# Kernel optimization log

Hardware: AMD Instinct MI355X
Metric: run time of the kernel (lower is better)

The kernel has to match this reference:

```python
import jax, jax.numpy as jnp
import numpy as np

B, D_IN, H, LAT = 4096, 4096, 4096, 512


def setup_inputs() -> dict:
    key = jax.random.key(0)
    ks = jax.random.split(key, 10)
    s = lambda fan_in: 1.0 / np.sqrt(fan_in)
    return {
        "x": jax.random.normal(ks[0], (B, D_IN), jnp.float32),
        "W_e1": jax.random.normal(ks[1], (D_IN, H), jnp.float32) * s(D_IN),
        "b_e1": jax.random.uniform(ks[2], (H,), jnp.float32),
        "W_e2": jax.random.normal(ks[3], (H, 2 * LAT), jnp.float32) * s(H),
        "b_e2": jax.random.uniform(ks[4], (2 * LAT,), jnp.float32),
        "W_d1": jax.random.normal(ks[5], (LAT, H), jnp.float32) * s(LAT),
        "b_d1": jax.random.uniform(ks[6], (H,), jnp.float32),
        "W_d2": jax.random.normal(ks[7], (H, D_IN), jnp.float32) * s(H),
        "b_d2": jax.random.uniform(ks[8], (D_IN,), jnp.float32),
        "eps": jax.random.normal(ks[9], (B, LAT), jnp.float32),
    }


def reference(x, W_e1, b_e1, W_e2, b_e2, W_d1, b_d1, W_d2, b_d2, eps):
    # encoder MLP
    h = jax.nn.relu(x @ W_e1 + b_e1)
    z = h @ W_e2 + b_e2                      # [B, 2*LAT]
    mu, logvar = z[:, :LAT], z[:, LAT:]
    # reparameterize: cholesky(diag(exp(logvar))) @ eps + mu == exp(0.5*logvar)*eps + mu
    zs = mu + jnp.exp(0.5 * logvar) * eps    # [B, LAT]
    # decoder MLP
    hd = jax.nn.relu(zs @ W_d1 + b_d1)
    recon = hd @ W_d2 + b_d2                 # [B, D_IN]
    return recon, mu, logvar
```

## Files before the change

### kernel.cpp

```cpp
#include <hip/hip_runtime.h>
#include <hip/hip_bf16.h>

typedef __attribute__((ext_vector_type(8))) __bf16 bf16x8;
typedef __attribute__((ext_vector_type(4))) float f32x4;
typedef __attribute__((ext_vector_type(4))) unsigned short ushort4v;
typedef __attribute__((ext_vector_type(8))) unsigned short ushort8v;
typedef unsigned short u16;

__device__ __forceinline__ u16 f2bf_bits(float f) {
    union { float f; unsigned int u; } x; x.f = f;
    unsigned int r = x.u + 0x7FFFu + ((x.u >> 16) & 1u);
    return (u16)(r >> 16);
}

__device__ __forceinline__ float bf2f(u16 u) {
    union { unsigned int i; float f; } x; x.i = ((unsigned)u) << 16; return x.f;
}

__device__ __forceinline__ void gload_lds16(const void* g, void* l) {
    __builtin_amdgcn_global_load_lds(
        (const __attribute__((address_space(1))) void*)g,
        (__attribute__((address_space(3))) void*)l, 16, 0, 0);
}

#define BARRIER()  __builtin_amdgcn_s_barrier()
#define LGKM0()    asm volatile("s_waitcnt lgkmcnt(0)" ::: "memory")
#define VMW8()     asm volatile("s_waitcnt vmcnt(8)" ::: "memory")

__global__ __launch_bounds__(256)
void prep(const float* __restrict__ x,   u16* __restrict__ xb,
          const float* __restrict__ We1, u16* __restrict__ w1t,
          const float* __restrict__ We2, u16* __restrict__ w2t,
          const float* __restrict__ Wd1, u16* __restrict__ w3t,
          const float* __restrict__ Wd2, u16* __restrict__ w4t) {
    int bid = blockIdx.x;

    if (bid >= 9728) {
        const int i = ((bid - 9728) << 10) + ((int)threadIdx.x << 2);
        f32x4 v = *reinterpret_cast<const f32x4*>(x + i);
        ushort4v o;
        o.x = f2bf_bits(v.x); o.y = f2bf_bits(v.y);
        o.z = f2bf_bits(v.z); o.w = f2bf_bits(v.w);
        *reinterpret_cast<ushort4v*>(xb + i) = o;
        return;
    }

    const float* in; u16* out; int R, C, bx, by;
    if (bid < 4096)      { in = We1; out = w1t; R = 4096; C = 4096; bx = bid & 63; by = bid >> 6; }
    else if (bid < 5120) { bid -= 4096; in = We2; out = w2t; R = 4096; C = 1024; bx = bid & 15; by = bid >> 4; }
    else if (bid < 5632) { bid -= 5120; in = Wd1; out = w3t; R = 512;  C = 4096; bx = bid & 63; by = bid >> 6; }
    else                 { bid -= 5632; in = Wd2; out = w4t; R = 4096; C = 4096; bx = bid & 63; by = bid >> 6; }

    __shared__ float t[64][67];
    const int c0 = bx << 6;
    const int r0 = by << 6;
    const int tx = threadIdx.x & 15;
    const int ty = threadIdx.x >> 4;
    #pragma unroll
    for (int j = 0; j < 4; ++j) {
        f32x4 v = *reinterpret_cast<const f32x4*>(
            &in[(size_t)(r0 + ty + 16 * j) * C + c0 + (tx << 2)]);
        *reinterpret_cast<f32x4*>(&t[ty + 16 * j][tx << 2]) = v;
    }
    __syncthreads();
    const int orow8 = threadIdx.x >> 3;
    const int seg8  = (threadIdx.x & 7) << 3;
    #pragma unroll
    for (int p = 0; p < 2; ++p) {
        const int oc = orow8 + (p << 5);
        ushort8v o;
        #pragma unroll
        for (int i = 0; i < 8; ++i)
            o[i] = f2bf_bits(t[seg8 + i][oc]);
        *reinterpret_cast<ushort8v*>(&out[(size_t)(c0 + oc) * R + r0 + seg8]) = o;
    }
}

__global__ __launch_bounds__(256)
void zred(const u16* __restrict__ P, const float* __restrict__ be2,
          const float* __restrict__ eps, float* __restrict__ mu,
          float* __restrict__ lv, u16* __restrict__ zs) {
    const int i = blockIdx.x * 256 + threadIdx.x;
    const int r = i >> 7;
    const int c4 = (i & 127) << 2;
    const size_t base = (size_t)r * 1024 + c4;
    const size_t PS = (size_t)4096 * 1024;

    f32x4 m = (f32x4)(0.0f);
    f32x4 l = (f32x4)(0.0f);
    #pragma unroll
    for (int s = 0; s < 4; ++s) {
        ushort4v pm = *reinterpret_cast<const ushort4v*>(P + s * PS + base);
        ushort4v pl = *reinterpret_cast<const ushort4v*>(P + s * PS + base + 512);
        m.x += bf2f(pm.x); m.y += bf2f(pm.y); m.z += bf2f(pm.z); m.w += bf2f(pm.w);
        l.x += bf2f(pl.x); l.y += bf2f(pl.y); l.z += bf2f(pl.z); l.w += bf2f(pl.w);
    }
    m += *reinterpret_cast<const f32x4*>(be2 + c4);
    l += *reinterpret_cast<const f32x4*>(be2 + 512 + c4);

    const size_t ob = (size_t)r * 512 + c4;
    *reinterpret_cast<f32x4*>(mu + ob) = m;
    *reinterpret_cast<f32x4*>(lv + ob) = l;

    f32x4 e = *reinterpret_cast<const f32x4*>(eps + ob);
    ushort4v o;
    o.x = f2bf_bits(m.x + __expf(0.5f * l.x) * e.x);
    o.y = f2bf_bits(m.y + __expf(0.5f * l.y) * e.y);
    o.z = f2bf_bits(m.z + __expf(0.5f * l.z) * e.z);
    o.w = f2bf_bits(m.w + __expf(0.5f * l.w) * e.w);
    *reinterpret_cast<ushort4v*>(zs + ob) = o;
}

template<int MODE, int PRIO>
__global__ __launch_bounds__(512, 2)
void gemm256(const u16* __restrict__ A, const u16* __restrict__ Bt,
             const float* __restrict__ bias,
             u16* __restrict__ obf, float* __restrict__ of32,
             int M, int N, int K, int ntiles)
{
    extern __shared__ char lds[];
    const int tid  = threadIdx.x;
    const int lane = tid & 63;
    const int w    = tid >> 6;
    const int wr   = w >> 2;
    const int wc   = w & 3;

    int bid = blockIdx.x;
    int sid = 0;
    int nwg = gridDim.x;
    if (MODE == 3) { sid = bid & 3; bid >>= 2; nwg >>= 2; }
    const int cpx = nwg >> 3;
    bid = (bid & 7) * cpx + (bid >> 3);
    const int nbx  = N >> 8;
    const int brow = (bid / nbx) << 8;
    const int bcol = (bid % nbx) << 8;
    const int kbase = (MODE == 3) ? sid * ntiles : 0;
    u16* pp = (MODE == 3) ? obf + (size_t)sid * M * N : obf;

    const int srow  = tid >> 3;
    const int scole = (((tid & 7) ^ (srow & 7)) << 4) >> 1;
    const size_t aoff = (size_t)(brow + srow) * K + scole;
    const size_t boff = (size_t)(bcol + srow) * K + scole;
    const size_t rowK64 = (size_t)64 * K;
    const int wave1024 = w << 10;

    const int lo16 = (lane >> 4) << 4;
    const int swzm = (lane & 7) << 4;
    const int low0 = lo16 ^ swzm;
    const int low1 = (64 | lo16) ^ swzm;
    const int rA   = (lane & 15) << 7;
    const int rB   = ((((wc & 1) << 6) | (lane & 15)) << 7);
    const int regA = wr << 14;
    const int regB = 32768 + ((wc >> 1) << 14);

    bf16x8 a[4][2];
    bf16x8 b0[2][2];
    bf16x8 b1[2][2];
    f32x4 acc[8][4];
    #pragma unroll
    for (int m = 0; m < 8; ++m)
        #pragma unroll
        for (int n = 0; n < 4; ++n)
            acc[m][n] = (f32x4)(0.0f);

#define STAGE_A(buf, h, kt) do { \
    const u16* _s = A + aoff + (size_t)(h) * 128 * K + (size_t)(kt) * 64; \
    gload_lds16(_s,          lds + ((buf) << 16) + ((h) << 14) + wave1024); \
    gload_lds16(_s + rowK64, lds + ((buf) << 16) + ((h) << 14) + 8192 + wave1024); \
} while (0)

#define STAGE_B(buf, h, kt) do { \
    const u16* _s = Bt + boff + (size_t)(h) * 128 * K + (size_t)(kt) * 64; \
    gload_lds16(_s,          lds + ((buf) << 16) + 32768 + ((h) << 14) + wave1024); \
    gload_lds16(_s + rowK64, lds + ((buf) << 16) + 32768 + ((h) << 14) + 8192 + wave1024); \
} while (0)

#define READ_A(buf, g) do { \
    _Pragma("unroll") \
    for (int m = 0; m < 4; ++m) { \
        const int _b = ((buf) << 16) + regA + rA + ((((g) << 2) + m) << 11); \
        a[m][0] = *reinterpret_cast<const bf16x8*>(lds + _b + low0); \
        a[m][1] = *reinterpret_cast<const bf16x8*>(lds + _b + low1); \
    } \
} while (0)

#define READ_B0(buf) do { \
    _Pragma("unroll") \
    for (int n = 0; n < 2; ++n) { \
        const int _b = ((buf) << 16) + regB + rB + (n << 11); \
        b0[n][0] = *reinterpret_cast<const bf16x8*>(lds + _b + low0); \
        b0[n][1] = *reinterpret_cast<const bf16x8*>(lds + _b + low1); \
    } \
} while (0)

#define READ_B1(buf) do { \
    _Pragma("unroll") \
    for (int n = 0; n < 2; ++n) { \
        const int _b = ((buf) << 16) + regB + rB + ((n + 2) << 11); \
        b1[n][0] = *reinterpret_cast<const bf16x8*>(lds + _b + low0); \
        b1[n][1] = *reinterpret_cast<const bf16x8*>(lds + _b + low1); \
    } \
} while (0)

#define MM(bx, mb, nb) do { \
    if (PRIO) __builtin_amdgcn_s_setprio(1); \
    _Pragma("unroll") \
    for (int m = 0; m < 4; ++m) \
        _Pragma("unroll") \
        for (int n = 0; n < 2; ++n) \
            _Pragma("unroll") \
            for (int s = 0; s < 2; ++s) \
                acc[(mb) + m][(nb) + n] = __builtin_amdgcn_mfma_f32_16x16x32_bf16( \
                    a[m][s], bx[n][s], acc[(mb) + m][(nb) + n], 0, 0, 0); \
    if (PRIO) __builtin_amdgcn_s_setprio(0); \
} while (0)

    const int NIT = ntiles >> 1;

    STAGE_A(0, 0, kbase); STAGE_A(0, 1, kbase); STAGE_B(0, 0, kbase); STAGE_B(0, 1, kbase);
    STAGE_A(1, 0, kbase + 1); STAGE_A(1, 1, kbase + 1); STAGE_B(1, 0, kbase + 1); STAGE_B(1, 1, kbase + 1);
    VMW8(); BARRIER();
    READ_A(0, 0); READ_B0(0);

    for (int it = 0; it < NIT; ++it) {
        const int tn0r = 2 * it + 2;
        const int tn1r = 2 * it + 3;
        const int tn0 = kbase + (tn0r < ntiles ? tn0r : ntiles - 1);
        const int tn1 = kbase + (tn1r < ntiles ? tn1r : ntiles - 1);

        BARRIER(); LGKM0();
        MM(b0, 0, 0);
        READ_B1(0);

        BARRIER(); LGKM0();
        STAGE_B(0, 0, tn0);
        MM(b1, 0, 2);
        READ_A(0, 1);

        BARRIER(); LGKM0();
        STAGE_B(0, 1, tn0);
        MM(b1, 4, 2);

        BARRIER(); LGKM0();
        STAGE_A(0, 0, tn0); STAGE_A(0, 1, tn0);
        MM(b0, 4, 0);
        VMW8();
        READ_A(1, 0); READ_B0(1);

        BARRIER(); LGKM0();
        MM(b0, 0, 0);
        READ_B1(1);

        BARRIER(); LGKM0();
        STAGE_B(1, 0, tn1);
        MM(b1, 0, 2);
        READ_A(1, 1);

        BARRIER(); LGKM0();
        STAGE_B(1, 1, tn1);
        MM(b1, 4, 2);

        BARRIER(); LGKM0();
        STAGE_A(1, 0, tn1); STAGE_A(1, 1, tn1);
        MM(b0, 4, 0);
        VMW8();
        READ_A(0, 0); READ_B0(0);
    }

    float bb[4];
    #pragma unroll
    for (int n = 0; n < 4; ++n)
        bb[n] = (MODE == 3) ? 0.0f : bias[bcol + (wc << 6) + (n << 4) + (lane & 15)];

    const int erow0 = brow + (wr << 7) + ((lane >> 4) << 2);
    const int ecol0 = bcol + (wc << 6) + (lane & 15);

    #pragma unroll
    for (int m = 0; m < 8; ++m) {
        #pragma unroll
        for (int i = 0; i < 4; ++i) {
            const int r = erow0 + (m << 4) + i;
            #pragma unroll
            for (int n = 0; n < 4; ++n) {
                const int c = ecol0 + (n << 4);
                float v = acc[m][n][i] + bb[n];
                if (MODE == 0) {
                    v = v > 0.0f ? v : 0.0f;
                    obf[(size_t)r * N + c] = f2bf_bits(v);
                } else if (MODE == 3) {
                    pp[(size_t)r * N + c] = f2bf_bits(v);
                } else {
                    of32[(size_t)r * N + c] = v;
                }
            }
        }
    }
#undef STAGE_A
#undef STAGE_B
#undef READ_A
#undef READ_B0
#undef READ_B1
#undef MM
}

extern "C" void kernel_launch(void* const* d_in, const int* in_sizes, int n_in,
                              void* d_out, int out_size, void* d_ws, size_t ws_size,
                              hipStream_t stream) {
    const float* x   = (const float*)d_in[0];
    const float* We1 = (const float*)d_in[1];
    const float* be1 = (const float*)d_in[2];
    const float* We2 = (const float*)d_in[3];
    const float* be2 = (const float*)d_in[4];
    const float* Wd1 = (const float*)d_in[5];
    const float* bd1 = (const float*)d_in[6];
    const float* Wd2 = (const float*)d_in[7];
    const float* bd2 = (const float*)d_in[8];
    const float* eps = (const float*)d_in[9];

    const int B = 4096, D = 4096, H = 4096, LAT = 512;

    char* ws = (char*)d_ws;
    u16*   xb    = (u16*)(ws);
    u16*   w1t   = (u16*)(ws + 33554432);
    u16*   w2t   = (u16*)(ws + 67108864);
    u16*   w3t   = (u16*)(ws + 75497472);
    u16*   w4t   = (u16*)(ws + 79691776);
    u16*   h     = (u16*)(ws + 113246208);
    u16*   part  = (u16*)(ws);
    u16*   zs    = (u16*)(ws + 113246208);
    u16*   hd    = (u16*)(ws);

    float* recon = (float*)d_out;
    float* mu    = recon + (size_t)B * D;
    float* lv    = mu + (size_t)B * LAT;

    hipFuncSetAttribute(reinterpret_cast<const void*>(gemm256<0, 0>),
                        hipFuncAttributeMaxDynamicSharedMemorySize, 131072);
    hipFuncSetAttribute(reinterpret_cast<const void*>(gemm256<0, 1>),
                        hipFuncAttributeMaxDynamicSharedMemorySize, 131072);
    hipFuncSetAttribute(reinterpret_cast<const void*>(gemm256<1, 1>),
                        hipFuncAttributeMaxDynamicSharedMemorySize, 131072);
    hipFuncSetAttribute(reinterpret_cast<const void*>(gemm256<3, 1>),
                        hipFuncAttributeMaxDynamicSharedMemorySize, 131072);

    prep<<<26112, 256, 0, stream>>>(x, xb, We1, w1t, We2, w2t, Wd1, w3t, Wd2, w4t);

    gemm256<0, 0><<<(B / 256) * (H / 256), 512, 131072, stream>>>(
        xb, w1t, be1, h, nullptr, B, H, D, D / 64);
    gemm256<3, 1><<<(B / 256) * (2 * LAT / 256) * 4, 512, 131072, stream>>>(
        h, w2t, nullptr, part, nullptr, B, 2 * LAT, H, (H / 64) / 4);
    zred<<<(B * LAT / 4) / 256, 256, 0, stream>>>(part, be2, eps, mu, lv, zs);
    gemm256<0, 1><<<(B / 256) * (H / 256), 512, 131072, stream>>>(
        zs, w3t, bd1, hd, nullptr, B, H, LAT, LAT / 64);
    gemm256<1, 1><<<(B / 256) * (D / 256), 512, 131072, stream>>>(
        hd, w4t, bd2, nullptr, recon, B, D, H, H / 64);
}
```

Measured before the change: 347.6 us.

## Double-buffer GEMM register fragments and interleave LDS reads with MFMAs

Fragment registers for A and B are duplicated so each phase can issue the LDS reads for the next phase before running its MFMAs, and sched_group_barrier hints ask the compiler to interleave DS reads with MFMA groups. The global-load wait is moved earlier and tightened to vmcnt(2), and the priority toggle is now applied to every GEMM, removing the PRIO template parameter. The aim is to hide LDS read latency behind matrix math. The extra fragment registers raise VGPR pressure at two blocks per CU, which may cause spills.

Result: slower. 418.1 us (+20.3%).

```diff
diff --git a/kernel.cpp b/kernel.cpp
--- a/kernel.cpp
+++ b/kernel.cpp
@@ -26,6 +26,9 @@
 #define BARRIER()  __builtin_amdgcn_s_barrier()
 #define LGKM0()    asm volatile("s_waitcnt lgkmcnt(0)" ::: "memory")
 #define VMW8()     asm volatile("s_waitcnt vmcnt(8)" ::: "memory")
+#define VMW2()     asm volatile("s_waitcnt vmcnt(2)" ::: "memory")
+#define SGB_DS(n)   __builtin_amdgcn_sched_group_barrier(0x100, n, 0)
+#define SGB_MFMA(n) __builtin_amdgcn_sched_group_barrier(0x8, n, 0)
 
 __global__ __launch_bounds__(256)
 void prep(const float* __restrict__ x,   u16* __restrict__ xb,
@@ -111,7 +114,7 @@
     *reinterpret_cast<ushort4v*>(zs + ob) = o;
 }
 
-template<int MODE, int PRIO>
+template<int MODE>
 __global__ __launch_bounds__(512, 2)
 void gemm256(const u16* __restrict__ A, const u16* __restrict__ Bt,
              const float* __restrict__ bias,
@@ -153,9 +156,9 @@
     const int regA = wr << 14;
     const int regB = 32768 + ((wc >> 1) << 14);
 
-    bf16x8 a[4][2];
-    bf16x8 b0[2][2];
-    bf16x8 b1[2][2];
+    bf16x8 aa0[4][2], aa1[4][2];
+    bf16x8 b0A[2][2], b0B[2][2];
+    bf16x8 b1A[2][2], b1B[2][2];
     f32x4 acc[8][4];
     #pragma unroll
     for (int m = 0; m < 8; ++m)
@@ -175,35 +178,26 @@
     gload_lds16(_s + rowK64, lds + ((buf) << 16) + 32768 + ((h) << 14) + 8192 + wave1024); \
 } while (0)
 
-#define READ_A(buf, g) do { \
+#define READ_AF(dst, buf, g) do { \
     _Pragma("unroll") \
     for (int m = 0; m < 4; ++m) { \
         const int _b = ((buf) << 16) + regA + rA + ((((g) << 2) + m) << 11); \
-        a[m][0] = *reinterpret_cast<const bf16x8*>(lds + _b + low0); \
-        a[m][1] = *reinterpret_cast<const bf16x8*>(lds + _b + low1); \
+        dst[m][0] = *reinterpret_cast<const bf16x8*>(lds + _b + low0); \
+        dst[m][1] = *reinterpret_cast<const bf16x8*>(lds + _b + low1); \
     } \
 } while (0)
 
-#define READ_B0(buf) do { \
+#define READ_BF(dst, buf, half) do { \
     _Pragma("unroll") \
     for (int n = 0; n < 2; ++n) { \
-        const int _b = ((buf) << 16) + regB + rB + (n << 11); \
-        b0[n][0] = *reinterpret_cast<const bf16x8*>(lds + _b + low0); \
-        b0[n][1] = *reinterpret_cast<const bf16x8*>(lds + _b + low1); \
+        const int _b = ((buf) << 16) + regB + rB + ((((half) << 1) + n) << 11); \
+        dst[n][0] = *reinterpret_cast<const bf16x8*>(lds + _b + low0); \
+        dst[n][1] = *reinterpret_cast<const bf16x8*>(lds + _b + low1); \
     } \
 } while (0)
 
-#define READ_B1(buf) do { \
-    _Pragma("unroll") \
-    for (int n = 0; n < 2; ++n) { \
-        const int _b = ((buf) << 16) + regB + rB + ((n + 2) << 11); \
-        b1[n][0] = *reinterpret_cast<const bf16x8*>(lds + _b + low0); \
-        b1[n][1] = *reinterpret_cast<const bf16x8*>(lds + _b + low1); \
-    } \
-} while (0)
-
-#define MM(bx, mb, nb) do { \
-    if (PRIO) __builtin_amdgcn_s_setprio(1); \
+#define MM_F(af, bf, mb, nb) do { \
+    __builtin_amdgcn_s_setprio(1); \
     _Pragma("unroll") \
     for (int m = 0; m < 4; ++m) \
         _Pragma("unroll") \
@@ -211,8 +205,8 @@
             _Pragma("unroll") \
             for (int s = 0; s < 2; ++s) \
                 acc[(mb) + m][(nb) + n] = __builtin_amdgcn_mfma_f32_16x16x32_bf16( \
-                    a[m][s], bx[n][s], acc[(mb) + m][(nb) + n], 0, 0, 0); \
-    if (PRIO) __builtin_amdgcn_s_setprio(0); \
+                    af[m][s], bf[n][s], acc[(mb) + m][(nb) + n], 0, 0, 0); \
+    __builtin_amdgcn_s_setprio(0); \
 } while (0)
 
     const int NIT = ntiles >> 1;
@@ -220,7 +214,7 @@
     STAGE_A(0, 0, kbase); STAGE_A(0, 1, kbase); STAGE_B(0, 0, kbase); STAGE_B(0, 1, kbase);
     STAGE_A(1, 0, kbase + 1); STAGE_A(1, 1, kbase + 1); STAGE_B(1, 0, kbase + 1); STAGE_B(1, 1, kbase + 1);
     VMW8(); BARRIER();
-    READ_A(0, 0); READ_B0(0);
+    READ_AF(aa0, 0, 0); READ_BF(b0A, 0, 0);
 
     for (int it = 0; it < NIT; ++it) {
         const int tn0r = 2 * it + 2;
@@ -229,42 +223,52 @@
         const int tn1 = kbase + (tn1r < ntiles ? tn1r : ntiles - 1);
 
         BARRIER(); LGKM0();
-        MM(b0, 0, 0);
-        READ_B1(0);
-
-        BARRIER(); LGKM0();
+        SGB_DS(4); SGB_MFMA(16);
+        READ_BF(b1A, 0, 1);
+        MM_F(aa0, b0A, 0, 0);
+
+        BARRIER(); LGKM0();
+        SGB_DS(8); SGB_MFMA(16);
+        READ_AF(aa1, 0, 1);
         STAGE_B(0, 0, tn0);
-        MM(b1, 0, 2);
-        READ_A(0, 1);
-
-        BARRIER(); LGKM0();
+        MM_F(aa0, b1A, 0, 2);
+        VMW2();
+
+        BARRIER(); LGKM0();
+        SGB_DS(8); SGB_MFMA(16);
+        READ_AF(aa0, 1, 0);
         STAGE_B(0, 1, tn0);
-        MM(b1, 4, 2);
-
-        BARRIER(); LGKM0();
+        MM_F(aa1, b1A, 4, 2);
+
+        BARRIER(); LGKM0();
+        SGB_DS(4); SGB_MFMA(16);
+        READ_BF(b0B, 1, 0);
         STAGE_A(0, 0, tn0); STAGE_A(0, 1, tn0);
-        MM(b0, 4, 0);
-        VMW8();
-        READ_A(1, 0); READ_B0(1);
-
-        BARRIER(); LGKM0();
-        MM(b0, 0, 0);
-        READ_B1(1);
-
-        BARRIER(); LGKM0();
+        MM_F(aa1, b0A, 4, 0);
+
+        BARRIER(); LGKM0();
+        SGB_DS(4); SGB_MFMA(16);
+        READ_BF(b1B, 1, 1);
+        MM_F(aa0, b0B, 0, 0);
+
+        BARRIER(); LGKM0();
+        SGB_DS(8); SGB_MFMA(16);
+        READ_AF(aa1, 1, 1);
         STAGE_B(1, 0, tn1);
-        MM(b1, 0, 2);
-        READ_A(1, 1);
-
-        BARRIER(); LGKM0();
+        MM_F(aa0, b1B, 0, 2);
+        VMW2();
+
+        BARRIER(); LGKM0();
+        SGB_DS(8); SGB_MFMA(16);
+        READ_AF(aa0, 0, 0);
         STAGE_B(1, 1, tn1);
-        MM(b1, 4, 2);
-
-        BARRIER(); LGKM0();
+        MM_F(aa1, b1B, 4, 2);
+
+        BARRIER(); LGKM0();
+        SGB_DS(4); SGB_MFMA(16);
+        READ_BF(b0A, 0, 0);
         STAGE_A(1, 0, tn1); STAGE_A(1, 1, tn1);
-        MM(b0, 4, 0);
-        VMW8();
-        READ_A(0, 0); READ_B0(0);
+        MM_F(aa1, b0B, 4, 0);
     }
 
     float bb[4];
@@ -297,10 +301,9 @@
     }
 #undef STAGE_A
 #undef STAGE_B
-#undef READ_A
-#undef READ_B0
-#undef READ_B1
-#undef MM
+#undef READ_AF
+#undef READ_BF
+#undef MM_F
 }
 
 extern "C" void kernel_launch(void* const* d_in, const int* in_sizes, int n_in,
@@ -334,24 +337,22 @@
     float* mu    = recon + (size_t)B * D;
     float* lv    = mu + (size_t)B * LAT;
 
-    hipFuncSetAttribute(reinterpret_cast<const void*>(gemm256<0, 0>),
+    hipFuncSetAttribute(reinterpret_cast<const void*>(gemm256<0>),
                         hipFuncAttributeMaxDynamicSharedMemorySize, 131072);
-    hipFuncSetAttribute(reinterpret_cast<const void*>(gemm256<0, 1>),
+    hipFuncSetAttribute(reinterpret_cast<const void*>(gemm256<1>),
                         hipFuncAttributeMaxDynamicSharedMemorySize, 131072);
-    hipFuncSetAttribute(reinterpret_cast<const void*>(gemm256<1, 1>),
+    hipFuncSetAttribute(reinterpret_cast<const void*>(gemm256<3>),
                         hipFuncAttributeMaxDynamicSharedMemorySize, 131072);
-    hipFuncSetAttribute(reinterpret_cast<const void*>(gemm256<3, 1>),
-                        hipFuncAttributeMaxDynamicSharedMemorySize, 131072);
 
     prep<<<26112, 256, 0, stream>>>(x, xb, We1, w1t, We2, w2t, Wd1, w3t, Wd2, w4t);
 
-    gemm256<0, 0><<<(B / 256) * (H / 256), 512, 131072, stream>>>(
+    gemm256<0><<<(B / 256) * (H / 256), 512, 131072, stream>>>(
         xb, w1t, be1, h, nullptr, B, H, D, D / 64);
-    gemm256<3, 1><<<(B / 256) * (2 * LAT / 256) * 4, 512, 131072, stream>>>(
+    gemm256<3><<<(B / 256) * (2 * LAT / 256) * 4, 512, 131072, stream>>>(
         h, w2t, nullptr, part, nullptr, B, 2 * LAT, H, (H / 64) / 4);
     zred<<<(B * LAT / 4) / 256, 256, 0, stream>>>(part, be2, eps, mu, lv, zs);
-    gemm256<0, 1><<<(B / 256) * (H / 256), 512, 131072, stream>>>(
+    gemm256<0><<<(B / 256) * (H / 256), 512, 131072, stream>>>(
         zs, w3t, bd1, hd, nullptr, B, H, LAT, LAT / 64);
-    gemm256<1, 1><<<(B / 256) * (D / 256), 512, 131072, stream>>>(
+    gemm256<1><<<(B / 256) * (D / 256), 512, 131072, stream>>>(
         hd, w4t, bd2, nullptr, recon, B, D, H, H / 64);
 }
```
